# Kernel optimization log

Measured on AMD Instinct MI355X. Metric: run time of the kernel, lower is better.

## Reference

```python
import jax, jax.numpy as jnp
import numpy as np

# Mamba dims: d_model=1024, expand=2 -> d_inner=2048, d_state=16, d_conv=4, dt_rank=ceil(1024/16)=64
B, L, D = 2, 1024, 1024
DIN, N, R, K = 2048, 16, 64, 4
LN_EPS = 1e-5


def setup_inputs():
    key = jax.random.key(0)
    ks = jax.random.split(key, 12)
    s = lambda fan_in: 1.0 / np.sqrt(fan_in)
    inp = {
        "x": jax.random.normal(ks[0], (B, L, D), jnp.float32),
        "W_in": jax.random.normal(ks[1], (D, 2 * DIN), jnp.float32) * s(D),
        "conv_w": jax.random.normal(ks[2], (DIN, K), jnp.float32) * s(K),
        "conv_b": jax.random.normal(ks[3], (DIN,), jnp.float32) * 0.02,
        "W_x": jax.random.normal(ks[4], (DIN, R + 2 * N), jnp.float32) * s(DIN),
        "W_dt": jax.random.normal(ks[5], (R, DIN), jnp.float32) * s(R),
        # bias chosen so softplus(bias) ~ small positive dt
        "b_dt": jnp.full((DIN,), -4.0, jnp.float32)
        + jax.random.normal(ks[6], (DIN,), jnp.float32) * 0.1,
        # S4D-real init: A = -[1..N] broadcast over channels
        "A_log": jnp.log(jnp.broadcast_to(jnp.arange(1, N + 1, dtype=jnp.float32), (DIN, N))),
        "D_skip": jnp.ones((DIN,), jnp.float32),
        "W_out": jax.random.normal(ks[7], (DIN, D), jnp.float32) * s(DIN),
        "ln_g": jnp.ones((D,), jnp.float32),
        "ln_b": jnp.zeros((D,), jnp.float32),
    }
    return inp


def _silu(x):
    return x * jax.nn.sigmoid(x)


def _mamba_forward(x, W_in, conv_w, conv_b, W_x, W_dt, b_dt, A_log, D_skip, W_out, ln_g, ln_b):
    # in_proj -> (x_in, z), each [B, L, DIN]
    xz = jnp.einsum("bld,de->ble", x, W_in)
    x_in, z = jnp.split(xz, 2, axis=-1)

    # causal depthwise conv1d (kernel K=4) via shifted sums
    xp = jnp.pad(x_in, ((0, 0), (K - 1, 0), (0, 0)))  # [B, L+K-1, DIN]
    x_conv = conv_b
    for k in range(K):
        x_conv = x_conv + xp[:, k : k + L, :] * conv_w[:, k]
    x_conv = _silu(x_conv)  # [B, L, DIN]

    # x_proj -> dt_rank + 2*N
    x_dbl = jnp.einsum("bld,de->ble", x_conv, W_x)
    dt, Bc, Cc = jnp.split(x_dbl, [R, R + N], axis=-1)  # [B,L,R], [B,L,N], [B,L,N]
    delta = jax.nn.softplus(jnp.einsum("blr,rd->bld", dt, W_dt) + b_dt)  # [B,L,DIN]

    A = -jnp.exp(A_log)  # [DIN, N]
    # discretize: deltaA [B,L,DIN,N], deltaB_u [B,L,DIN,N]
    deltaA = jnp.exp(delta[..., None] * A)
    deltaBu = delta[..., None] * Bc[:, :, None, :] * x_conv[..., None]

    # selective scan over time
    def step(h, inp):
        dA, dBu, C_t = inp  # [B,DIN,N], [B,DIN,N], [B,N]
        h = dA * h + dBu
        y_t = jnp.einsum("bdn,bn->bd", h, C_t)
        return h, y_t

    h0 = jnp.zeros((B, DIN, N), jnp.float32)
    xs = (
        jnp.moveaxis(deltaA, 1, 0),
        jnp.moveaxis(deltaBu, 1, 0),
        jnp.moveaxis(Cc, 1, 0),
    )
    _, ys = jax.lax.scan(step, h0, xs)  # ys: [L, B, DIN]
    y = jnp.moveaxis(ys, 0, 1) + x_conv * D_skip  # [B, L, DIN]

    y = y * _silu(z)
    out = jnp.einsum("bld,de->ble", y, W_out)  # [B, L, D]

    # post LayerNorm
    mu = jnp.mean(out, axis=-1, keepdims=True)
    var = jnp.mean(jnp.square(out - mu), axis=-1, keepdims=True)
    return (out - mu) * jax.lax.rsqrt(var + LN_EPS) * ln_g + ln_b


def reference(x, W_in, conv_w, conv_b, W_x, W_dt, b_dt, A_log, D_skip, W_out, ln_g, ln_b):
    return _mamba_forward(x, W_in, conv_w, conv_b, W_x, W_dt, b_dt, A_log, D_skip, W_out, ln_g, ln_b)
```

## Files before the change

kernel.cpp:

```cpp
#include <hip/hip_runtime.h>

#define LSEQ 1024
#define DMODEL 1024
#define DINNER 2048
#define NSTATE 16
#define RRANK 64
#define CHUNK 32
#define NCHUNK 32
#define KSPLIT 8
#define MF (1024 * 1024)

typedef unsigned short u16;
typedef __attribute__((ext_vector_type(8))) short bf16x8;
typedef __attribute__((ext_vector_type(4))) short bf16x4;
typedef __attribute__((ext_vector_type(4))) float f32x4;

__device__ __forceinline__ float sigmoidf_(float x) {
    return 1.0f / (1.0f + __expf(-x));
}
__device__ __forceinline__ float softplusf_(float x) {
    return (x > 20.0f) ? x : log1pf(__expf(x));
}
__device__ __forceinline__ short f2bf(float f) {
    union { float f; unsigned u; } v; v.f = f;
    unsigned r = v.u + 0x7FFF + ((v.u >> 16) & 1);
    return (short)(r >> 16);
}
__device__ __forceinline__ float bf2f(u16 b) {
    union { unsigned u; float f; } v; v.u = ((unsigned)b) << 16;
    return v.f;
}
__device__ __forceinline__ void async_cp16(const u16* g, u16* l) {
    __builtin_amdgcn_global_load_lds(
        (const __attribute__((address_space(1))) unsigned int*)g,
        (__attribute__((address_space(3))) unsigned int*)l, 16, 0, 0);
}

__global__ __launch_bounds__(256) void cast_all_kernel(
    const float* __restrict__ x, u16* __restrict__ xb,
    const float* __restrict__ Win, u16* __restrict__ Wbin,
    const float* __restrict__ Wout, u16* __restrict__ Wbout)
{
    __shared__ float t[32][33];
    int bid = blockIdx.x;
    if (bid < 1024) {
        const size_t i = ((size_t)bid * 256 + threadIdx.x) * 8;
        float4 a = *(const float4*)&x[i];
        float4 b = *(const float4*)&x[i + 4];
        bf16x8 o;
        o[0] = f2bf(a.x); o[1] = f2bf(a.y); o[2] = f2bf(a.z); o[3] = f2bf(a.w);
        o[4] = f2bf(b.x); o[5] = f2bf(b.y); o[6] = f2bf(b.z); o[7] = f2bf(b.w);
        *(bf16x8*)&xb[i] = o;
        return;
    }
    const float* in; u16* out; int R, C, bxi, byi;
    if (bid < 1024 + 4096) {
        int tt = bid - 1024;
        in = Win; out = Wbin; R = DMODEL; C = 2 * DINNER;
        bxi = tt & 127; byi = tt >> 7;
    } else {
        int tt = bid - 5120;
        in = Wout; out = Wbout; R = DINNER; C = DMODEL;
        bxi = tt & 31; byi = tt >> 5;
    }
    const int bx = bxi * 32, by = byi * 32;
    const int tx = threadIdx.x & 31, ty = threadIdx.x >> 5;
    #pragma unroll
    for (int i = 0; i < 4; ++i)
        t[ty + 8 * i][tx] = in[(size_t)(by + ty + 8 * i) * C + bx + tx];
    __syncthreads();
    #pragma unroll
    for (int i = 0; i < 4; ++i)
        out[(size_t)(bx + ty + 8 * i) * R + by + tx] = (u16)f2bf(t[tx][ty + 8 * i]);
}

template<int BM, int BN, int BK, int KSPL, bool BF16OUT>
__global__ __launch_bounds__(256) void mfma_gemm_kernel(
    const u16* __restrict__ A, const u16* __restrict__ Bt,
    float* __restrict__ Cf, u16* __restrict__ Cb, int M, int N, int K)
{
    constexpr int WMS = BM / 32;
    constexpr int WNS = BN / 32;
    __shared__ u16 lA[BM * BK];
    __shared__ u16 lB[BN * BK];

    const int tid  = threadIdx.x;
    const int lane = tid & 63, wave = tid >> 6;
    const int quad = lane >> 4, l16 = lane & 15;
    const int wm   = (wave >> 1) * (BM / 2);
    const int wn   = (wave & 1) * (BN / 2);
    const int row0 = blockIdx.y * BM;
    const int col0 = blockIdx.x * BN;
    const int Kz   = K / KSPL;
    const int kbeg = blockIdx.z * Kz;

    f32x4 acc[WMS][WNS];
    #pragma unroll
    for (int i = 0; i < WMS; ++i)
        #pragma unroll
        for (int j = 0; j < WNS; ++j)
            acc[i][j] = (f32x4){0.f, 0.f, 0.f, 0.f};

    for (int k0 = kbeg; k0 < kbeg + Kz; k0 += BK) {
        #pragma unroll
        for (int t = 0; t < (BM * BK) / 2048; ++t) {
            int c = tid + t * 256;
            int r = c / (BK / 8), kc = c % (BK / 8);
            async_cp16(&A[(size_t)(row0 + r) * K + k0 + kc * 8], &lA[c * 8]);
        }
        #pragma unroll
        for (int t = 0; t < (BN * BK) / 2048; ++t) {
            int c = tid + t * 256;
            int r = c / (BK / 8), kc = c % (BK / 8);
            async_cp16(&Bt[(size_t)(col0 + r) * K + k0 + kc * 8], &lB[c * 8]);
        }
        __syncthreads();
        #pragma unroll
        for (int ks = 0; ks < BK; ks += 32) {
            bf16x8 af[WMS], bfr[WNS];
            #pragma unroll
            for (int i = 0; i < WMS; ++i)
                af[i] = *(bf16x8*)&lA[(wm + i * 16 + l16) * BK + ks + quad * 8];
            #pragma unroll
            for (int j = 0; j < WNS; ++j)
                bfr[j] = *(bf16x8*)&lB[(wn + j * 16 + l16) * BK + ks + quad * 8];
            #pragma unroll
            for (int i = 0; i < WMS; ++i)
                #pragma unroll
                for (int j = 0; j < WNS; ++j)
                    acc[i][j] = __builtin_amdgcn_mfma_f32_16x16x32_bf16(
                        af[i], bfr[j], acc[i][j], 0, 0, 0);
        }
        __syncthreads();
    }
    if (BF16OUT) {
        #pragma unroll
        for (int i = 0; i < WMS; ++i)
            #pragma unroll
            for (int j = 0; j < WNS; ++j)
                #pragma unroll
                for (int r = 0; r < 4; ++r)
                    Cb[(size_t)(row0 + wm + i * 16 + quad * 4 + r) * N
                       + col0 + wn + j * 16 + l16] = (u16)f2bf(acc[i][j][r]);
    } else {
        float* Cp = Cf + (size_t)blockIdx.z * M * N;
        #pragma unroll
        for (int i = 0; i < WMS; ++i)
            #pragma unroll
            for (int j = 0; j < WNS; ++j)
                #pragma unroll
                for (int r = 0; r < 4; ++r)
                    Cp[(size_t)(row0 + wm + i * 16 + quad * 4 + r) * N
                       + col0 + wn + j * 16 + l16] = acc[i][j][r];
    }
}

__global__ __launch_bounds__(256) void conv_silu_kernel(
    const u16* __restrict__ XZb, const float* __restrict__ cw,
    const float* __restrict__ cb, u16* __restrict__ xcb)
{
    const int idx = blockIdx.x * 256 + threadIdx.x;
    const int dq  = idx % (DINNER / 4);
    const int bl  = idx / (DINNER / 4);
    const int l   = bl % LSEQ;
    const int d0  = dq * 4;

    const float4* cw4 = (const float4*)cw;
    const float4 W0 = cw4[d0 + 0];
    const float4 W1 = cw4[d0 + 1];
    const float4 W2 = cw4[d0 + 2];
    const float4 W3 = cw4[d0 + 3];
    float4 s = *(const float4*)&cb[d0];

    #pragma unroll
    for (int k = 0; k < 4; ++k) {
        int ls = l + k - 3;
        if (ls >= 0) {
            bf16x4 xv = *(const bf16x4*)&XZb[(size_t)(bl + k - 3) * (2 * DINNER) + d0];
            s.x = fmaf(bf2f((u16)xv[0]), ((const float*)&W0)[k], s.x);
            s.y = fmaf(bf2f((u16)xv[1]), ((const float*)&W1)[k], s.y);
            s.z = fmaf(bf2f((u16)xv[2]), ((const float*)&W2)[k], s.z);
            s.w = fmaf(bf2f((u16)xv[3]), ((const float*)&W3)[k], s.w);
        }
    }
    bf16x4 o;
    o[0] = f2bf(s.x * sigmoidf_(s.x));
    o[1] = f2bf(s.y * sigmoidf_(s.y));
    o[2] = f2bf(s.z * sigmoidf_(s.z));
    o[3] = f2bf(s.w * sigmoidf_(s.w));
    *(bf16x4*)&xcb[(size_t)idx * 4] = o;
}

__global__ __launch_bounds__(256) void xproj_part_kernel(
    const u16* __restrict__ xcb, const float* __restrict__ Wx,
    float* __restrict__ part)
{
    __shared__ float As[32][64 + 4];
    __shared__ float Ws[32][96 + 4];

    const int tid  = threadIdx.x;
    const int tx   = tid % 32;
    const int ty   = tid / 32;
    const int row0 = blockIdx.x * 64;
    const int k0   = blockIdx.y * (DINNER / KSPLIT);

    float acc[8][3];
    #pragma unroll
    for (int i = 0; i < 8; ++i) { acc[i][0] = 0.f; acc[i][1] = 0.f; acc[i][2] = 0.f; }

    for (int kt = 0; kt < DINNER / KSPLIT; kt += 32) {
        const int kb = k0 + kt;
        {
            int m = tid >> 2, kq = tid & 3;
            bf16x8 v = *(const bf16x8*)&xcb[(size_t)(row0 + m) * DINNER + kb + kq * 8];
            #pragma unroll
            for (int j = 0; j < 8; ++j)
                As[kq * 8 + j][m] = bf2f((u16)v[j]);
        }
        #pragma unroll
        for (int i = 0; i < 3; ++i) {
            int lin = tid + i * 256;
            int kk = lin / 24, q = lin % 24;
            *(float4*)&Ws[kk][q * 4] = *(const float4*)&Wx[(size_t)(kb + kk) * 96 + q * 4];
        }
        __syncthreads();
        #pragma unroll 8
        for (int kk = 0; kk < 32; ++kk) {
            float a[8];
            *(float4*)&a[0] = *(const float4*)&As[kk][ty * 8];
            *(float4*)&a[4] = *(const float4*)&As[kk][ty * 8 + 4];
            float b0 = Ws[kk][tx], b1 = Ws[kk][tx + 32], b2 = Ws[kk][tx + 64];
            #pragma unroll
            for (int i = 0; i < 8; ++i) {
                acc[i][0] = fmaf(a[i], b0, acc[i][0]);
                acc[i][1] = fmaf(a[i], b1, acc[i][1]);
                acc[i][2] = fmaf(a[i], b2, acc[i][2]);
            }
        }
        __syncthreads();
    }
    float* po = part + (size_t)blockIdx.y * (2 * LSEQ * 96);
    #pragma unroll
    for (int i = 0; i < 8; ++i) {
        int r = row0 + ty * 8 + i;
        po[(size_t)r * 96 + tx]      = acc[i][0];
        po[(size_t)r * 96 + tx + 32] = acc[i][1];
        po[(size_t)r * 96 + tx + 64] = acc[i][2];
    }
}

__global__ __launch_bounds__(256) void delta_fused_kernel(
    const float* __restrict__ part, const float* __restrict__ Wdt,
    const float* __restrict__ bdt, u16* __restrict__ deltab,
    float* __restrict__ xBC)
{
    __shared__ float As[64][64 + 4];
    __shared__ float Ws[64][64 + 4];
    const int tid  = threadIdx.x;
    const int tx   = tid % 16;
    const int ty   = tid / 16;
    const int row0 = blockIdx.y * 64;
    const int col0 = blockIdx.x * 64;

    #pragma unroll
    for (int i = 0; i < 4; ++i) {
        int lin = tid + i * 256;
        int m = lin / 16, kq = lin % 16;
        float4 v = {0.f, 0.f, 0.f, 0.f};
        #pragma unroll
        for (int s8 = 0; s8 < KSPLIT; ++s8) {
            float4 p = *(const float4*)&part[(size_t)s8 * (2 * LSEQ * 96)
                                             + (size_t)(row0 + m) * 96 + kq * 4];
            v.x += p.x; v.y += p.y; v.z += p.z; v.w += p.w;
        }
        As[kq * 4 + 0][m] = v.x;
        As[kq * 4 + 1][m] = v.y;
        As[kq * 4 + 2][m] = v.z;
        As[kq * 4 + 3][m] = v.w;
    }
    #pragma unroll
    for (int i = 0; i < 4; ++i) {
        int lin = tid + i * 256;
        int kk = lin / 16, q = lin % 16;
        *(float4*)&Ws[kk][q * 4] = *(const float4*)&Wdt[(size_t)kk * DINNER + col0 + q * 4];
    }
    __syncthreads();

    float acc[4][4];
    #pragma unroll
    for (int i = 0; i < 4; ++i)
        #pragma unroll
        for (int j = 0; j < 4; ++j) acc[i][j] = 0.0f;

    #pragma unroll 8
    for (int kk = 0; kk < 64; ++kk) {
        float4 a = *(const float4*)&As[kk][ty * 4];
        float4 b = *(const float4*)&Ws[kk][tx * 4];
        const float* ap = (const float*)&a;
        const float* bp = (const float*)&b;
        #pragma unroll
        for (int i = 0; i < 4; ++i)
            #pragma unroll
            for (int j = 0; j < 4; ++j)
                acc[i][j] = fmaf(ap[i], bp[j], acc[i][j]);
    }

    float4 bv = *(const float4*)&bdt[col0 + tx * 4];
    const float* bvp = (const float*)&bv;
    #pragma unroll
    for (int i = 0; i < 4; ++i) {
        bf16x4 o;
        o[0] = f2bf(softplusf_(acc[i][0] + bvp[0]));
        o[1] = f2bf(softplusf_(acc[i][1] + bvp[1]));
        o[2] = f2bf(softplusf_(acc[i][2] + bvp[2]));
        o[3] = f2bf(softplusf_(acc[i][3] + bvp[3]));
        *(bf16x4*)&deltab[(size_t)(row0 + ty * 4 + i) * DINNER + col0 + tx * 4] = o;
    }

    if (blockIdx.x == 0) {
        #pragma unroll
        for (int i = 0; i < 8; ++i) {
            int lin = tid + i * 256;
            int r = lin >> 5, c2 = lin & 31;
            float s = 0.0f;
            #pragma unroll
            for (int s8 = 0; s8 < KSPLIT; ++s8)
                s += part[(size_t)s8 * (2 * LSEQ * 96)
                          + (size_t)(row0 + r) * 96 + RRANK + c2];
            xBC[(size_t)(row0 + r) * 32 + c2] = s;
        }
    }
}

__global__ __launch_bounds__(256) void scan_part1_kernel(
    const u16* __restrict__ deltab, const u16* __restrict__ xcb,
    const float* __restrict__ xBC, const float* __restrict__ A_log,
    float* __restrict__ Pbuf, float* __restrict__ Hbuf)
{
    const int d  = blockIdx.x * 256 + threadIdx.x;
    const int b  = blockIdx.y;
    const int ch = blockIdx.z;

    float Aa[NSTATE];
    #pragma unroll
    for (int q = 0; q < 4; ++q) {
        float4 v = *(const float4*)&A_log[(size_t)d * NSTATE + q * 4];
        Aa[q * 4 + 0] = -__expf(v.x);
        Aa[q * 4 + 1] = -__expf(v.y);
        Aa[q * 4 + 2] = -__expf(v.z);
        Aa[q * 4 + 3] = -__expf(v.w);
    }
    float h[NSTATE], P[NSTATE];
    #pragma unroll
    for (int n = 0; n < NSTATE; ++n) { h[n] = 0.0f; P[n] = 1.0f; }

    const size_t row0 = (size_t)b * LSEQ + (size_t)ch * CHUNK;
    #pragma unroll 4
    for (int t = 0; t < CHUNK; ++t) {
        const size_t row = row0 + t;
        float dv  = bf2f(deltab[row * DINNER + d]);
        float xcv = bf2f(xcb[row * DINNER + d]);
        float du  = dv * xcv;
        const float4* br = (const float4*)&xBC[row * 32];
        float4 B4[4] = { br[0], br[1], br[2], br[3] };
        const float* Bv = (const float*)B4;
        #pragma unroll
        for (int n = 0; n < NSTATE; ++n) {
            float dA = __expf(dv * Aa[n]);
            h[n] = fmaf(dA, h[n], du * Bv[n]);
            P[n] *= dA;
        }
    }
    float* Pp = &Pbuf[(((size_t)ch * 2 + b) * DINNER + d) * NSTATE];
    float* Hp = &Hbuf[(((size_t)ch * 2 + b) * DINNER + d) * NSTATE];
    #pragma unroll
    for (int q = 0; q < 4; ++q) {
        *(float4*)&Pp[q * 4] = *(float4*)&P[q * 4];
        *(float4*)&Hp[q * 4] = *(float4*)&h[q * 4];
    }
}

__global__ __launch_bounds__(256) void scan_combine_kernel(
    const float* __restrict__ Pbuf, const float* __restrict__ Hbuf,
    float* __restrict__ h0buf)
{
    const int idx = blockIdx.x * 256 + threadIdx.x;
    float H = 0.0f;
    #pragma unroll 8
    for (int cch = 0; cch < NCHUNK; ++cch) {
        const size_t g = (size_t)cch * (2 * DINNER * NSTATE) + idx;
        h0buf[g] = H;
        H = fmaf(Pbuf[g], H, Hbuf[g]);
    }
}

__global__ __launch_bounds__(256) void scan_part2_kernel(
    const u16* __restrict__ deltab, const u16* __restrict__ xcb,
    const float* __restrict__ xBC, const float* __restrict__ h0buf,
    const u16* __restrict__ XZb, u16* __restrict__ yb,
    const float* __restrict__ A_log, const float* __restrict__ Dskip)
{
    const int d  = blockIdx.x * 256 + threadIdx.x;
    const int b  = blockIdx.y;
    const int ch = blockIdx.z;

    float Aa[NSTATE];
    #pragma unroll
    for (int q = 0; q < 4; ++q) {
        float4 v = *(const float4*)&A_log[(size_t)d * NSTATE + q * 4];
        Aa[q * 4 + 0] = -__expf(v.x);
        Aa[q * 4 + 1] = -__expf(v.y);
        Aa[q * 4 + 2] = -__expf(v.z);
        Aa[q * 4 + 3] = -__expf(v.w);
    }
    const float Dd = Dskip[d];

    float h[NSTATE];
    const float* Hp = &h0buf[(((size_t)ch * 2 + b) * DINNER + d) * NSTATE];
    #pragma unroll
    for (int q = 0; q < 4; ++q)
        *(float4*)&h[q * 4] = *(const float4*)&Hp[q * 4];

    const size_t row0 = (size_t)b * LSEQ + (size_t)ch * CHUNK;
    #pragma unroll 2
    for (int t = 0; t < CHUNK; ++t) {
        const size_t row = row0 + t;
        float dv  = bf2f(deltab[row * DINNER + d]);
        float xcv = bf2f(xcb[row * DINNER + d]);
        float du  = dv * xcv;
        const float4* br = (const float4*)&xBC[row * 32];
        float4 BC[8] = { br[0], br[1], br[2], br[3], br[4], br[5], br[6], br[7] };
        const float* Bv = (const float*)BC;
        const float* Cv = Bv + NSTATE;
        float y = 0.0f;
        #pragma unroll
        for (int n = 0; n < NSTATE; ++n) {
            float dA = __expf(dv * Aa[n]);
            h[n] = fmaf(dA, h[n], du * Bv[n]);
            y = fmaf(h[n], Cv[n], y);
        }
        float zz = bf2f(XZb[row * (2 * DINNER) + DINNER + d]);
        float yv = (y + xcv * Dd) * (zz * sigmoidf_(zz));
        yb[row * DINNER + d] = (u16)f2bf(yv);
    }
}

__global__ __launch_bounds__(256) void ln4_kernel(
    const float* __restrict__ p, const float* __restrict__ g,
    const float* __restrict__ b, float* __restrict__ out)
{
    const int row = blockIdx.x;
    const int tid = threadIdx.x;
    const size_t off = (size_t)row * DMODEL + tid * 4;
    float4 v0 = *(const float4*)&p[off];
    float4 v1 = *(const float4*)&p[off + 2 * MF];
    float4 v2 = *(const float4*)&p[off + 4 * (size_t)MF];
    float4 v3 = *(const float4*)&p[off + 6 * (size_t)MF];
    float4 v;
    v.x = (v0.x + v1.x) + (v2.x + v3.x);
    v.y = (v0.y + v1.y) + (v2.y + v3.y);
    v.z = (v0.z + v1.z) + (v2.z + v3.z);
    v.w = (v0.w + v1.w) + (v2.w + v3.w);
    float s = v.x + v.y + v.z + v.w;
    float q = v.x * v.x + v.y * v.y + v.z * v.z + v.w * v.w;
    #pragma unroll
    for (int m = 1; m < 64; m <<= 1) {
        s += __shfl_xor(s, m, 64);
        q += __shfl_xor(q, m, 64);
    }
    __shared__ float ss[4], qq[4];
    if ((tid & 63) == 0) { ss[tid >> 6] = s; qq[tid >> 6] = q; }
    __syncthreads();
    float S = ss[0] + ss[1] + ss[2] + ss[3];
    float Q = qq[0] + qq[1] + qq[2] + qq[3];
    float mu  = S * (1.0f / DMODEL);
    float var = Q * (1.0f / DMODEL) - mu * mu;
    float rs  = rsqrtf(var + 1e-5f);
    float4 gv = *(const float4*)&g[tid * 4];
    float4 bv = *(const float4*)&b[tid * 4];
    float4 o;
    o.x = (v.x - mu) * rs * gv.x + bv.x;
    o.y = (v.y - mu) * rs * gv.y + bv.y;
    o.z = (v.z - mu) * rs * gv.z + bv.z;
    o.w = (v.w - mu) * rs * gv.w + bv.w;
    *(float4*)&out[(size_t)row * DMODEL + tid * 4] = o;
}

extern "C" void kernel_launch(void* const* d_in, const int* in_sizes, int n_in,
                              void* d_out, int out_size, void* d_ws, size_t ws_size,
                              hipStream_t stream) {
    const float* x      = (const float*)d_in[0];
    const float* W_in   = (const float*)d_in[1];
    const float* conv_w = (const float*)d_in[2];
    const float* conv_b = (const float*)d_in[3];
    const float* W_x    = (const float*)d_in[4];
    const float* W_dt   = (const float*)d_in[5];
    const float* b_dt   = (const float*)d_in[6];
    const float* A_log  = (const float*)d_in[7];
    const float* D_skip = (const float*)d_in[8];
    const float* W_out  = (const float*)d_in[9];
    const float* ln_g   = (const float*)d_in[10];
    const float* ln_b   = (const float*)d_in[11];
    (void)in_sizes; (void)n_in; (void)out_size; (void)ws_size;

    const int M = 2 * LSEQ;

    float* ws     = (float*)d_ws;
    u16*   XZb    = (u16*)ws;
    u16*   xcb    = (u16*)(ws + 4 * MF);
    u16*   deltab = (u16*)(ws + 6 * MF);
    float* part   = ws + 8 * (size_t)MF;
    float* Pbuf   = ws + 8 * (size_t)MF;
    float* Hbuf   = ws + 10 * (size_t)MF;
    float* h0     = ws + 12 * (size_t)MF;
    u16*   xb     = (u16*)(ws + 14 * MF);
    u16*   Wbin   = (u16*)(ws + 15 * MF);
    u16*   Wbout  = (u16*)(ws + 17 * MF);
    float* xBC    = ws + 18 * (size_t)MF;
    u16*   yb     = (u16*)(ws + 15 * MF);
    float* pout   = ws;

    cast_all_kernel<<<1024 + 4096 + 2048, 256, 0, stream>>>(
        x, xb, W_in, Wbin, W_out, Wbout);

    mfma_gemm_kernel<128, 128, 64, 1, true>
        <<<dim3((2 * DINNER) / 128, M / 128, 1), 256, 0, stream>>>(
            xb, Wbin, nullptr, XZb, M, 2 * DINNER, DMODEL);

    conv_silu_kernel<<<(M * (DINNER / 4)) / 256, 256, 0, stream>>>(
        XZb, conv_w, conv_b, xcb);

    xproj_part_kernel<<<dim3(M / 64, KSPLIT), 256, 0, stream>>>(xcb, W_x, part);

    delta_fused_kernel<<<dim3(DINNER / 64, M / 64), 256, 0, stream>>>(
        part, W_dt, b_dt, deltab, xBC);

    scan_part1_kernel<<<dim3(DINNER / 256, 2, NCHUNK), 256, 0, stream>>>(
        deltab, xcb, xBC, A_log, Pbuf, Hbuf);
    scan_combine_kernel<<<(2 * DINNER * NSTATE) / 256, 256, 0, stream>>>(
        Pbuf, Hbuf, h0);
    scan_part2_kernel<<<dim3(DINNER / 256, 2, NCHUNK), 256, 0, stream>>>(
        deltab, xcb, xBC, h0, XZb, yb, A_log, D_skip);

    mfma_gemm_kernel<128, 128, 64, 4, false>
        <<<dim3(DMODEL / 128, M / 128, 4), 256, 0, stream>>>(
            yb, Wbout, pout, nullptr, M, DMODEL, DINNER);

    ln4_kernel<<<M, 256, 0, stream>>>(pout, ln_g, ln_b, (float*)d_out);
}
```

Baseline: 277.7 us.

## Replace out-proj split-K with 64x64 tiles and add XCD-aware block swizzle

Drops the 4-way split-K on the output projection GEMM and uses 64x64 tiles with full-K accumulation, so the LayerNorm kernel reads one result buffer instead of summing four partials. Both GEMMs also remap block IDs in groups of eight, intended to give each XCD-local group contiguous tiles for better L2 reuse. The out-proj GEMM now launches 512 blocks, each running a longer serial K loop with smaller tiles and less operand reuse per tile.

```diff
diff --git a/kernel.cpp b/kernel.cpp
--- a/kernel.cpp
+++ b/kernel.cpp
@@ -74,7 +74,7 @@
         out[(size_t)(bx + ty + 8 * i) * R + by + tx] = (u16)f2bf(t[tx][ty + 8 * i]);
 }
 
-template<int BM, int BN, int BK, int KSPL, bool BF16OUT>
+template<int BM, int BN, int BK, bool BF16OUT, int SWZ>
 __global__ __launch_bounds__(256) void mfma_gemm_kernel(
     const u16* __restrict__ A, const u16* __restrict__ Bt,
     float* __restrict__ Cf, u16* __restrict__ Cb, int M, int N, int K)
@@ -89,10 +89,17 @@
     const int quad = lane >> 4, l16 = lane & 15;
     const int wm   = (wave >> 1) * (BM / 2);
     const int wn   = (wave & 1) * (BN / 2);
-    const int row0 = blockIdx.y * BM;
-    const int col0 = blockIdx.x * BN;
-    const int Kz   = K / KSPL;
-    const int kbeg = blockIdx.z * Kz;
+
+    const int gx = gridDim.x, gy = gridDim.y;
+    const int id = blockIdx.x + gx * blockIdx.y;
+    const int G8 = (gx * gy) >> 3;
+    const int id2 = (id & 7) * G8 + (id >> 3);
+    int bx, by;
+    if (SWZ == 1)      { bx = id2 / gy; by = id2 % gy; }
+    else if (SWZ == 2) { by = id2 / gx; bx = id2 % gx; }
+    else               { bx = blockIdx.x; by = blockIdx.y; }
+    const int row0 = by * BM;
+    const int col0 = bx * BN;
 
     f32x4 acc[WMS][WNS];
     #pragma unroll
@@ -101,7 +108,7 @@
         for (int j = 0; j < WNS; ++j)
             acc[i][j] = (f32x4){0.f, 0.f, 0.f, 0.f};
 
-    for (int k0 = kbeg; k0 < kbeg + Kz; k0 += BK) {
+    for (int k0 = 0; k0 < K; k0 += BK) {
         #pragma unroll
         for (int t = 0; t < (BM * BK) / 2048; ++t) {
             int c = tid + t * 256;
@@ -143,14 +150,13 @@
                     Cb[(size_t)(row0 + wm + i * 16 + quad * 4 + r) * N
                        + col0 + wn + j * 16 + l16] = (u16)f2bf(acc[i][j][r]);
     } else {
-        float* Cp = Cf + (size_t)blockIdx.z * M * N;
         #pragma unroll
         for (int i = 0; i < WMS; ++i)
             #pragma unroll
             for (int j = 0; j < WNS; ++j)
                 #pragma unroll
                 for (int r = 0; r < 4; ++r)
-                    Cp[(size_t)(row0 + wm + i * 16 + quad * 4 + r) * N
+                    Cf[(size_t)(row0 + wm + i * 16 + quad * 4 + r) * N
                        + col0 + wn + j * 16 + l16] = acc[i][j][r];
     }
 }
@@ -445,22 +451,13 @@
     }
 }
 
-__global__ __launch_bounds__(256) void ln4_kernel(
-    const float* __restrict__ p, const float* __restrict__ g,
+__global__ __launch_bounds__(256) void ln_kernel(
+    const float* __restrict__ t, const float* __restrict__ g,
     const float* __restrict__ b, float* __restrict__ out)
 {
     const int row = blockIdx.x;
     const int tid = threadIdx.x;
-    const size_t off = (size_t)row * DMODEL + tid * 4;
-    float4 v0 = *(const float4*)&p[off];
-    float4 v1 = *(const float4*)&p[off + 2 * MF];
-    float4 v2 = *(const float4*)&p[off + 4 * (size_t)MF];
-    float4 v3 = *(const float4*)&p[off + 6 * (size_t)MF];
-    float4 v;
-    v.x = (v0.x + v1.x) + (v2.x + v3.x);
-    v.y = (v0.y + v1.y) + (v2.y + v3.y);
-    v.z = (v0.z + v1.z) + (v2.z + v3.z);
-    v.w = (v0.w + v1.w) + (v2.w + v3.w);
+    float4 v = *(const float4*)&t[(size_t)row * DMODEL + tid * 4];
     float s = v.x + v.y + v.z + v.w;
     float q = v.x * v.x + v.y * v.y + v.z * v.z + v.w * v.w;
     #pragma unroll
@@ -523,8 +520,8 @@
     cast_all_kernel<<<1024 + 4096 + 2048, 256, 0, stream>>>(
         x, xb, W_in, Wbin, W_out, Wbout);
 
-    mfma_gemm_kernel<128, 128, 64, 1, true>
-        <<<dim3((2 * DINNER) / 128, M / 128, 1), 256, 0, stream>>>(
+    mfma_gemm_kernel<128, 128, 64, true, 1>
+        <<<dim3((2 * DINNER) / 128, M / 128), 256, 0, stream>>>(
             xb, Wbin, nullptr, XZb, M, 2 * DINNER, DMODEL);
 
     conv_silu_kernel<<<(M * (DINNER / 4)) / 256, 256, 0, stream>>>(
@@ -542,9 +539,9 @@
     scan_part2_kernel<<<dim3(DINNER / 256, 2, NCHUNK), 256, 0, stream>>>(
         deltab, xcb, xBC, h0, XZb, yb, A_log, D_skip);
 
-    mfma_gemm_kernel<128, 128, 64, 4, false>
-        <<<dim3(DMODEL / 128, M / 128, 4), 256, 0, stream>>>(
+    mfma_gemm_kernel<64, 64, 64, false, 2>
+        <<<dim3(DMODEL / 64, M / 64), 256, 0, stream>>>(
             yb, Wbout, pout, nullptr, M, DMODEL, DINNER);
 
-    ln4_kernel<<<M, 256, 0, stream>>>(pout, ln_g, ln_b, (float*)d_out);
-}
+    ln_kernel<<<M, 256, 0, stream>>>(pout, ln_g, ln_b, (float*)d_out);
+}
```

Result: slower. 283.8 us (+2.2%).
